# Kernel tuning notes

Measured on AMD Instinct MI355X. Metric: run time of the kernel, lower is better.

The kernel has to match this reference:

```python
import jax, jax.numpy as jnp
import numpy as np

NUM_HEADS = 16

def setup_inputs() -> dict:
    key = jax.random.key(0)
    k1, k2 = jax.random.split(key)
    x = jax.random.normal(k1, (4, 4096, 1024), dtype=jnp.float32)
    # nn.Linear(dim, 3*dim, bias=False) weight: [3*dim, dim]
    w_qkv = jax.random.normal(k2, (3072, 1024), dtype=jnp.float32) * (1024 ** -0.5)
    return {"x": x, "w_qkv": w_qkv}

def reference(x, w_qkv):
    B, N, C = x.shape
    H = NUM_HEADS
    d = C // H
    # qkv projection: [B,N,3C] -> [3,B,H,N,d]
    qkv = jnp.einsum('bnc,oc->bno', x, w_qkv)
    qkv = qkv.reshape(B, N, 3, H, d).transpose(2, 0, 3, 1, 4)
    q, k, v = qkv[0], qkv[1], qkv[2]
    q = jax.nn.softmax(q, axis=-1) * (d ** -0.5)  # softmax over head_dim, then scale
    k = jax.nn.softmax(k, axis=-2)                # softmax over sequence dim
    context = jnp.einsum('bhnd,bhne->bhde', k, v)  # [B,H,d,d]
    out = jnp.einsum('bhnd,bhde->bhne', q, context)  # [B,H,N,d]
    return out
```

## Files before the change

### kernel.cpp

```cpp
#include <hip/hip_runtime.h>
#include <stdint.h>

typedef __attribute__((ext_vector_type(4))) float f32x4;
typedef __attribute__((ext_vector_type(8))) __bf16 bf16x8;
typedef unsigned short u16;

#define AS1 __attribute__((address_space(1)))
#define AS3 __attribute__((address_space(3)))

__device__ __forceinline__ u16 f2bf(float f) {
  uint32_t u = __float_as_uint(f);
  u += 0x7fffu + ((u >> 16) & 1u);
  return (u16)(u >> 16);
}
__device__ __forceinline__ float bf2f(u16 s) {
  return __uint_as_float(((uint32_t)s) << 16);
}

__device__ __forceinline__ void gload_lds16(const void* g, void* l) {
  __builtin_amdgcn_global_load_lds((const AS1 void*)g, (AS3 void*)l, 16, 0, 0);
}

__device__ __forceinline__ bf16x8 ones_bf16x8() {
  uint32_t o4[4] = {0x3F803F80u, 0x3F803F80u, 0x3F803F80u, 0x3F803F80u};
  return *(bf16x8*)o4;
}


__global__ __launch_bounds__(256) void cvt_all(const float* __restrict__ X,
                                               const float* __restrict__ W,
                                               u16* __restrict__ x16,
                                               u16* __restrict__ w16,
                                               float* __restrict__ ctxbase) {
  const int gb = blockIdx.x;
  if (gb >= 9728) {
    const int idx = (gb - 9728) * 256 + threadIdx.x;
    for (int i = idx; i < 66560; i += 1024)
      ((f32x4*)ctxbase)[i] = (f32x4){0.f, 0.f, 0.f, 0.f};
    return;
  }
  const float* src;
  u16* dst;
  int i;
  if (gb < 8192) {
    src = X; dst = x16; i = gb * 256 + threadIdx.x;
  } else {
    src = W; dst = w16; i = (gb - 8192) * 256 + threadIdx.x;
  }
  const f32x4 a = ((const f32x4*)src)[2 * i];
  const f32x4 b = ((const f32x4*)src)[2 * i + 1];
  ushort4 lo, hi;
  lo.x = f2bf(a.x); lo.y = f2bf(a.y); lo.z = f2bf(a.z); lo.w = f2bf(a.w);
  hi.x = f2bf(b.x); hi.y = f2bf(b.y); hi.z = f2bf(b.z); hi.w = f2bf(b.w);
  ((ushort4*)dst)[2 * i] = lo;
  ((ushort4*)dst)[2 * i + 1] = hi;
}

__global__ __launch_bounds__(512, 2) void qkv_gemm(const u16* __restrict__ X,
                                                   const u16* __restrict__ W,
                                                   float* __restrict__ QOUT,
                                                   u16* __restrict__ KV) {
  __shared__ __attribute__((aligned(16))) u16 lds[8 * 128 * 64];

  const int t = threadIdx.x;
  const int D = blockIdx.x;
  const int xcd = D & 7;
  const int s = D >> 3;
  const int otile = s % 12;
  const int mtile = (s / 12) * 8 + xcd;
  const int oblk = otile << 8;
  const int mblk = mtile << 8;

  const int wv = t >> 6;
  const int l = t & 63;
  const int wm = wv >> 2;
  const int wnx = wv & 3;
  const int l15 = l & 15;
  const int lq = l >> 4;
  const int sp = t & 7;

  char* ldsc = (char*)lds;

  auto stageA = [&](int tau, int h, int par) {
#pragma unroll
    for (int j = 0; j < 2; j++) {
      const int ur = (j << 6) | (t >> 3);
      const int R = ((ur >> 6) << 7) | (h << 6) | (ur & 63);
      const u16* g = X + (size_t)(mblk + R) * 1024 + (tau << 6) +
                     ((sp ^ (ur & 7)) << 3);
      gload_lds16(g, ldsc + (((par << 2) | h) << 14) + (((j << 9) | t) << 4));
    }
  };
  auto stageB = [&](int tau, int h, int par) {
#pragma unroll
    for (int j = 0; j < 2; j++) {
      const int ur = (j << 6) | (t >> 3);
      const int R = ((ur >> 5) << 6) | (h << 5) | (ur & 31);
      const u16* g = W + (size_t)(oblk + R) * 1024 + (tau << 6) +
                     ((sp ^ (ur & 7)) << 3);
      gload_lds16(g,
                  ldsc + (((par << 2) | 2 | h) << 14) + (((j << 9) | t) << 4));
    }
  };

  const int co0 = (((l >> 4) ^ (l & 7)) << 4);
  const int co1 = ((((l >> 4) | 4) ^ (l & 7)) << 4);
  const int aOff = ((wm << 6) | l15) << 7;
  const int bOff = ((wnx << 5) | l15) << 7;

  bf16x8 bA[2][4], bL[2][2], bH[2][2];
  auto loadA = [&](int h, int par) {
    const char* base = ldsc + (((par << 2) | h) << 14) + aOff;
#pragma unroll
    for (int fm = 0; fm < 4; fm++) {
      bA[0][fm] = *(const bf16x8*)(base + (fm << 11) + co0);
      bA[1][fm] = *(const bf16x8*)(base + (fm << 11) + co1);
    }
  };
  auto loadB2 = [&](int nh, int par, bf16x8(&bb)[2][2]) {
    const char* base = ldsc + (((par << 2) | 2 | nh) << 14) + bOff;
#pragma unroll
    for (int fn = 0; fn < 2; fn++) {
      bb[0][fn] = *(const bf16x8*)(base + (fn << 11) + co0);
      bb[1][fn] = *(const bf16x8*)(base + (fn << 11) + co1);
    }
  };

  f32x4 acc[8][4];
#pragma unroll
  for (int i = 0; i < 8; i++)
#pragma unroll
    for (int j = 0; j < 4; j++) acc[i][j] = (f32x4){0.f, 0.f, 0.f, 0.f};

  auto mfma16 = [&](int ah, int nh, bf16x8(&bb)[2][2]) {
#pragma unroll
    for (int fm = 0; fm < 4; fm++)
#pragma unroll
      for (int fn = 0; fn < 2; fn++)
#pragma unroll
        for (int ks = 0; ks < 2; ks++)
          acc[(ah << 2) | fm][(nh << 1) | fn] =
              __builtin_amdgcn_mfma_f32_16x16x32_bf16(
                  bA[ks][fm], bb[ks][fn], acc[(ah << 2) | fm][(nh << 1) | fn],
                  0, 0, 0);
  };

  stageA(0, 0, 0);
  stageA(0, 1, 0);
  stageB(0, 0, 0);
  stageB(0, 1, 0);
  stageA(1, 0, 1);
  stageB(1, 1, 1);
  asm volatile("s_waitcnt vmcnt(4)" ::: "memory");
  __builtin_amdgcn_s_barrier();

#pragma unroll 1
  for (int tau = 0; tau < 16; tau++) {
    const int par = tau & 1;
    loadA(0, par);
    loadB2(0, par, bL);
    if (tau < 15) stageA(tau + 1, 1, par ^ 1);
    asm volatile("s_waitcnt lgkmcnt(0)" ::: "memory");
    __builtin_amdgcn_s_setprio(1);
    mfma16(0, 0, bL);
    __builtin_amdgcn_s_setprio(0);
    __builtin_amdgcn_s_barrier();
    loadB2(1, par, bH);
    if (tau < 15) stageB(tau + 1, 0, par ^ 1);
    asm volatile("s_waitcnt lgkmcnt(0)" ::: "memory");
    __builtin_amdgcn_s_setprio(1);
    mfma16(0, 1, bH);
    __builtin_amdgcn_s_setprio(0);
    __builtin_amdgcn_s_barrier();
    loadA(1, par);
    if (tau < 14) stageA(tau + 2, 0, par);
    asm volatile("s_waitcnt lgkmcnt(0)" ::: "memory");
    __builtin_amdgcn_s_setprio(1);
    mfma16(1, 1, bH);
    __builtin_amdgcn_s_setprio(0);
    __builtin_amdgcn_s_barrier();
    if (tau < 14) stageB(tau + 2, 1, par);
    __builtin_amdgcn_s_setprio(1);
    mfma16(1, 0, bL);
    __builtin_amdgcn_s_setprio(0);
    if (tau < 14) {
      asm volatile("s_waitcnt vmcnt(4)" ::: "memory");
    } else if (tau == 14) {
      asm volatile("s_waitcnt vmcnt(0)" ::: "memory");
    }
    __builtin_amdgcn_s_barrier();
  }

  const bool is_q = (oblk < 1024);
  if (is_q) {
    float* LF = (float*)lds;
#pragma unroll 1
    for (int hh = 0; hh < 2; hh++) {
      __syncthreads();
      if (wm == hh) {
#pragma unroll
        for (int fm = 0; fm < 8; fm++) {
#pragma unroll
          for (int fn = 0; fn < 4; fn++) {
            const int colq = ((wnx << 2) | fn);
#pragma unroll
            for (int r = 0; r < 4; r++) {
              const int row = (fm << 4) + (lq << 2) + r;
              const int g = colq ^ lq;
              LF[(row << 8) + (g << 4) + l15] = acc[fm][fn][r];
            }
          }
        }
      }
      __syncthreads();
      const int nbase = mblk + (hh << 7);
#pragma unroll
      for (int p = 0; p < 16; p++) {
        const int u = (p << 9) + t;
        const int row = u >> 6;
        const int c = u & 63;
        const int g = (c >> 2) ^ ((row >> 2) & 3);
        const f32x4 v4 = *(const f32x4*)&LF[(row << 8) + (g << 4) + ((c & 3) << 2)];
        const int rowg = nbase + row;
        const int bq = rowg >> 12, n = rowg & 4095;
        const int head = (oblk >> 6) + (c >> 4);
        *(f32x4*)&QOUT[((((size_t)((bq << 4) + head)) << 12) + n) * 64 +
                       ((c & 15) << 2)] = v4;
      }
    }
  } else {
    u16* ks = KV + (((size_t)((mtile << 3) + (otile - 4))) << 16) + (wv << 13) +
              (l << 2);
#pragma unroll
    for (int fm = 0; fm < 8; fm++) {
#pragma unroll
      for (int fn = 0; fn < 4; fn++) {
        ushort4 sv;
        sv.x = f2bf(acc[fm][fn][0]);
        sv.y = f2bf(acc[fm][fn][1]);
        sv.z = f2bf(acc[fm][fn][2]);
        sv.w = f2bf(acc[fm][fn][3]);
        *(ushort4*)(ks + (((fm << 2) | fn) << 8)) = sv;
      }
    }
  }
}

__global__ __launch_bounds__(256) void ctx_colsum(const u16* __restrict__ KV,
                                                  float* __restrict__ ctxraw,
                                                  float* __restrict__ colsum) {
  __shared__ __attribute__((aligned(16))) u16 ekT[64 * 128];
  __shared__ __attribute__((aligned(16))) u16 evT[64 * 128];

  const int t = threadIdx.x;
  const int bh = blockIdx.y;
  const int b = bh >> 4, h = bh & 15;
  const int sgrp = blockIdx.x;
  const int w = t >> 6;
  const int l = t & 63;
  const int l15 = l & 15;
  const int lk = l >> 4;
  const int lq = (t >> 4) & 3;
  const int d_st = (w << 4) | l15;

  uint2 kr[8], vr[8];
  auto issue = [&](int it) {
    const int mt = (b << 4) + (sgrp << 2) + (it >> 1);
    const int wmb = it & 1;
    const size_t base = ((size_t)((mt << 3) + (h >> 2)) << 16) |
                        ((size_t)wmb << 15) | ((size_t)(h & 3) << 13) |
                        (size_t)(t << 2);
#pragma unroll
    for (int fm = 0; fm < 8; fm++) {
      kr[fm] = *(const uint2*)(KV + base + (fm << 10));
      vr[fm] = *(const uint2*)(KV + base + (fm << 10) + (4 << 16));
    }
  };
  auto stage = [&]() {
#pragma unroll
    for (int fm = 0; fm < 8; fm++) {
      const int c = (fm << 1) | (lq >> 1);
      const int off = (d_st << 8) + ((c ^ (d_st & 7)) << 4) + ((lq & 1) << 3);
      ushort4 es;
      es.x = f2bf(__expf(bf2f((u16)(kr[fm].x & 0xffff))));
      es.y = f2bf(__expf(bf2f((u16)(kr[fm].x >> 16))));
      es.z = f2bf(__expf(bf2f((u16)(kr[fm].y & 0xffff))));
      es.w = f2bf(__expf(bf2f((u16)(kr[fm].y >> 16))));
      *(ushort4*)((char*)ekT + off) = es;
      *(uint2*)((char*)evT + off) = vr[fm];
    }
  };

  f32x4 acc[4], acc1[4];
#pragma unroll
  for (int i = 0; i < 4; i++) {
    acc[i] = (f32x4){0.f, 0.f, 0.f, 0.f};
    acc1[i] = (f32x4){0.f, 0.f, 0.f, 0.f};
  }
  const bf16x8 ones = ones_bf16x8();
  const int eo = (w << 4) | l15;

  issue(0);
#pragma unroll 1
  for (int it = 0; it < 8; it++) {
    stage();
    if (it < 7) issue(it + 1);
    __syncthreads();
#pragma unroll
    for (int ksx = 0; ksx < 4; ksx++) {
      const bf16x8 bfrag = *(const bf16x8*)(
          (char*)evT + (eo << 8) + ((((ksx << 2) | lk) ^ (eo & 7)) << 4));
#pragma unroll
      for (int fmA = 0; fmA < 4; fmA++) {
        const int dA = (fmA << 4) | l15;
        const bf16x8 afrag = *(const bf16x8*)(
            (char*)ekT + (dA << 8) + ((((ksx << 2) | lk) ^ (dA & 7)) << 4));
        acc[fmA] = __builtin_amdgcn_mfma_f32_16x16x32_bf16(afrag, bfrag,
                                                           acc[fmA], 0, 0, 0);
        if (w == 0)
          acc1[fmA] = __builtin_amdgcn_mfma_f32_16x16x32_bf16(afrag, ones,
                                                              acc1[fmA], 0, 0, 0);
      }
    }
    __syncthreads();
  }

  float* dst = ctxraw + ((size_t)bh << 12);
#pragma unroll
  for (int fmA = 0; fmA < 4; fmA++)
#pragma unroll
    for (int r = 0; r < 4; r++) {
      const int d = (fmA << 4) + (lk << 2) + r;
      atomicAdd(&dst[(d << 6) + eo], acc[fmA][r]);
    }
  if (w == 0 && l15 == 0) {
#pragma unroll
    for (int fmA = 0; fmA < 4; fmA++)
#pragma unroll
      for (int r = 0; r < 4; r++) {
        const int d = (fmA << 4) + (lk << 2) + r;
        atomicAdd(&colsum[(bh << 6) + d], acc1[fmA][r]);
      }
  }
}

__global__ __launch_bounds__(256) void out_kernel(const float* __restrict__ ctxraw,
                                                  const float* __restrict__ colsum,
                                                  float* __restrict__ OUT) {
  __shared__ __attribute__((aligned(16))) u16 qe[256 * 64];
  __shared__ __attribute__((aligned(16))) u16 ctxT[64 * 64];

  const int t = threadIdx.x;
  const int bh = blockIdx.y;
  const int n0 = blockIdx.x << 8;
  const float* craw = ctxraw + ((size_t)bh << 12);
  float* qbase = OUT + ((size_t)bh * 4096 + n0) * 64;

#pragma unroll
  for (int p = 0; p < 4; p++) {
    const int vi = (p << 8) + t;
    const int d = vi >> 4;
    const int e4 = (vi & 15) << 2;
    const f32x4 cv = *(const f32x4*)(craw + (vi << 2));
    const float inv = 1.0f / colsum[(bh << 6) + d];
#pragma unroll
    for (int j = 0; j < 4; j++) {
      const int e = e4 + j;
      *(u16*)((char*)ctxT + (e << 7) + (((d >> 3) ^ (e & 7)) << 4) +
              ((d & 7) << 1)) = f2bf(cv[j] * inv);
    }
  }
#pragma unroll
  for (int p = 0; p < 16; p++) {
    const int idx = (p << 8) + t;
    const int row = idx >> 4;
    const int c4 = idx & 15;
    const f32x4 qv = *(const f32x4*)(qbase + (row << 6) + (c4 << 2));
    ushort4 ev;
    ev.x = f2bf(__expf(qv.x));
    ev.y = f2bf(__expf(qv.y));
    ev.z = f2bf(__expf(qv.z));
    ev.w = f2bf(__expf(qv.w));
    *(ushort4*)((char*)qe + (row << 7) + (((c4 >> 1) ^ (row & 7)) << 4) +
                ((c4 & 1) << 3)) = ev;
  }
  __syncthreads();

  const int w = t >> 6;
  const int l = t & 63;
  const int l15 = l & 15;
  const int lk = l >> 4;

  f32x4 acc[4][4], acc1[4];
#pragma unroll
  for (int i = 0; i < 4; i++) {
    acc1[i] = (f32x4){0.f, 0.f, 0.f, 0.f};
#pragma unroll
    for (int j = 0; j < 4; j++) acc[i][j] = (f32x4){0.f, 0.f, 0.f, 0.f};
  }
  const bf16x8 ones = ones_bf16x8();

#pragma unroll
  for (int ksx = 0; ksx < 2; ksx++) {
    bf16x8 bfr[4];
#pragma unroll
    for (int fn = 0; fn < 4; fn++) {
      const int e = (fn << 4) | l15;
      bfr[fn] = *(const bf16x8*)((char*)ctxT + (e << 7) +
                                 ((((ksx << 2) | lk) ^ (e & 7)) << 4));
    }
#pragma unroll
    for (int fm = 0; fm < 4; fm++) {
      const int row = (w << 6) | (fm << 4) | l15;
      const bf16x8 afr = *(const bf16x8*)(
          (char*)qe + (row << 7) + ((((ksx << 2) | lk) ^ (row & 7)) << 4));
      acc1[fm] = __builtin_amdgcn_mfma_f32_16x16x32_bf16(afr, ones, acc1[fm],
                                                         0, 0, 0);
#pragma unroll
      for (int fn = 0; fn < 4; fn++)
        acc[fm][fn] = __builtin_amdgcn_mfma_f32_16x16x32_bf16(afr, bfr[fn],
                                                              acc[fm][fn], 0, 0, 0);
    }
  }

#pragma unroll
  for (int fm = 0; fm < 4; fm++) {
#pragma unroll
    for (int r = 0; r < 4; r++) {
      const int row = (w << 6) + (fm << 4) + (lk << 2) + r;
      const float inv = 0.125f / acc1[fm][r];
#pragma unroll
      for (int fn = 0; fn < 4; fn++)
        qbase[(row << 6) + (fn << 4) + l15] = acc[fm][fn][r] * inv;
    }
  }
}

extern "C" void kernel_launch(void* const* d_in, const int* in_sizes, int n_in,
                              void* d_out, int out_size, void* d_ws, size_t ws_size,
                              hipStream_t stream) {
  const float* Xf = (const float*)d_in[0];
  const float* Wf = (const float*)d_in[1];

  u16* x16 = (u16*)d_ws;
  u16* w16 = x16 + (size_t)16384 * 1024;
  u16* KV = w16 + (size_t)3072 * 1024;
  float* ctxraw = (float*)(KV + (size_t)16384 * 2048);
  float* colsum = ctxraw + 64 * 64 * 64;
  float* QOUT = (float*)d_out;

  cvt_all<<<dim3(9732), 256, 0, stream>>>(Xf, Wf, x16, w16, ctxraw);
  qkv_gemm<<<dim3(768), 512, 0, stream>>>(x16, w16, QOUT, KV);
  ctx_colsum<<<dim3(4, 64), 256, 0, stream>>>(KV, ctxraw, colsum);
  out_kernel<<<dim3(16, 64), 256, 0, stream>>>(ctxraw, colsum, QOUT);
}
```

Measured before the change: 264.7 us.

## Load GEMM B operand directly from global into registers, halve LDS footprint

The QKV GEMM no longer stages the weight tile through LDS. Each wave now loads its B fragments straight from global memory into registers, and only the X tile is double-buffered in shared memory, which halves the LDS allocation. The main loop drops most of its barriers and waits. The Q epilogue is reorganized into four 64-row passes so it fits the smaller LDS. The aim is more occupancy and less LDS traffic and synchronization, at the cost of uncoalesced, unswizzled global loads for W and a full vmcnt(0) wait every iteration, which exposes latency.

```diff
diff --git a/kernel.cpp b/kernel.cpp
--- a/kernel.cpp
+++ b/kernel.cpp
@@ -60,7 +60,7 @@
                                                    const u16* __restrict__ W,
                                                    float* __restrict__ QOUT,
                                                    u16* __restrict__ KV) {
-  __shared__ __attribute__((aligned(16))) u16 lds[8 * 128 * 64];
+  __shared__ __attribute__((aligned(16))) u16 lds[4 * 128 * 64];
 
   const int t = threadIdx.x;
   const int D = blockIdx.x;
@@ -88,41 +88,30 @@
       const int R = ((ur >> 6) << 7) | (h << 6) | (ur & 63);
       const u16* g = X + (size_t)(mblk + R) * 1024 + (tau << 6) +
                      ((sp ^ (ur & 7)) << 3);
-      gload_lds16(g, ldsc + (((par << 2) | h) << 14) + (((j << 9) | t) << 4));
-    }
-  };
-  auto stageB = [&](int tau, int h, int par) {
-#pragma unroll
-    for (int j = 0; j < 2; j++) {
-      const int ur = (j << 6) | (t >> 3);
-      const int R = ((ur >> 5) << 6) | (h << 5) | (ur & 31);
-      const u16* g = W + (size_t)(oblk + R) * 1024 + (tau << 6) +
-                     ((sp ^ (ur & 7)) << 3);
-      gload_lds16(g,
-                  ldsc + (((par << 2) | 2 | h) << 14) + (((j << 9) | t) << 4));
-    }
+      gload_lds16(g, ldsc + (((par << 1) | h) << 14) + (((j << 9) | t) << 4));
+    }
+  };
+
+  auto loadBg = [&](int tau, int nh, bf16x8(&bb)[2][2]) {
+    const u16* base = W + (size_t)(oblk + (wnx << 6) + (nh << 5) + l15) * 1024 +
+                      (tau << 6) + (lq << 3);
+    bb[0][0] = *(const bf16x8*)(base);
+    bb[0][1] = *(const bf16x8*)(base + 16 * 1024);
+    bb[1][0] = *(const bf16x8*)(base + 32);
+    bb[1][1] = *(const bf16x8*)(base + 16 * 1024 + 32);
   };
 
   const int co0 = (((l >> 4) ^ (l & 7)) << 4);
   const int co1 = ((((l >> 4) | 4) ^ (l & 7)) << 4);
   const int aOff = ((wm << 6) | l15) << 7;
-  const int bOff = ((wnx << 5) | l15) << 7;
 
   bf16x8 bA[2][4], bL[2][2], bH[2][2];
   auto loadA = [&](int h, int par) {
-    const char* base = ldsc + (((par << 2) | h) << 14) + aOff;
+    const char* base = ldsc + (((par << 1) | h) << 14) + aOff;
 #pragma unroll
     for (int fm = 0; fm < 4; fm++) {
       bA[0][fm] = *(const bf16x8*)(base + (fm << 11) + co0);
       bA[1][fm] = *(const bf16x8*)(base + (fm << 11) + co1);
-    }
-  };
-  auto loadB2 = [&](int nh, int par, bf16x8(&bb)[2][2]) {
-    const char* base = ldsc + (((par << 2) | 2 | nh) << 14) + bOff;
-#pragma unroll
-    for (int fn = 0; fn < 2; fn++) {
-      bb[0][fn] = *(const bf16x8*)(base + (fn << 11) + co0);
-      bb[1][fn] = *(const bf16x8*)(base + (fn << 11) + co1);
     }
   };
 
@@ -147,47 +136,32 @@
 
   stageA(0, 0, 0);
   stageA(0, 1, 0);
-  stageB(0, 0, 0);
-  stageB(0, 1, 0);
-  stageA(1, 0, 1);
-  stageB(1, 1, 1);
-  asm volatile("s_waitcnt vmcnt(4)" ::: "memory");
+  loadBg(0, 0, bL);
+  asm volatile("s_waitcnt vmcnt(0)" ::: "memory");
   __builtin_amdgcn_s_barrier();
 
 #pragma unroll 1
   for (int tau = 0; tau < 16; tau++) {
     const int par = tau & 1;
+    if (tau < 15) {
+      stageA(tau + 1, 0, par ^ 1);
+      stageA(tau + 1, 1, par ^ 1);
+    }
+    loadBg(tau, 1, bH);
     loadA(0, par);
-    loadB2(0, par, bL);
-    if (tau < 15) stageA(tau + 1, 1, par ^ 1);
-    asm volatile("s_waitcnt lgkmcnt(0)" ::: "memory");
     __builtin_amdgcn_s_setprio(1);
     mfma16(0, 0, bL);
-    __builtin_amdgcn_s_setprio(0);
-    __builtin_amdgcn_s_barrier();
-    loadB2(1, par, bH);
-    if (tau < 15) stageB(tau + 1, 0, par ^ 1);
-    asm volatile("s_waitcnt lgkmcnt(0)" ::: "memory");
-    __builtin_amdgcn_s_setprio(1);
     mfma16(0, 1, bH);
     __builtin_amdgcn_s_setprio(0);
-    __builtin_amdgcn_s_barrier();
     loadA(1, par);
-    if (tau < 14) stageA(tau + 2, 0, par);
-    asm volatile("s_waitcnt lgkmcnt(0)" ::: "memory");
+    __builtin_amdgcn_s_setprio(1);
+    mfma16(1, 0, bL);
+    __builtin_amdgcn_s_setprio(0);
+    if (tau < 15) loadBg(tau + 1, 0, bL);
     __builtin_amdgcn_s_setprio(1);
     mfma16(1, 1, bH);
     __builtin_amdgcn_s_setprio(0);
-    __builtin_amdgcn_s_barrier();
-    if (tau < 14) stageB(tau + 2, 1, par);
-    __builtin_amdgcn_s_setprio(1);
-    mfma16(1, 0, bL);
-    __builtin_amdgcn_s_setprio(0);
-    if (tau < 14) {
-      asm volatile("s_waitcnt vmcnt(4)" ::: "memory");
-    } else if (tau == 14) {
-      asm volatile("s_waitcnt vmcnt(0)" ::: "memory");
-    }
+    asm volatile("s_waitcnt vmcnt(0)" ::: "memory");
     __builtin_amdgcn_s_barrier();
   }
 
@@ -195,28 +169,29 @@
   if (is_q) {
     float* LF = (float*)lds;
 #pragma unroll 1
-    for (int hh = 0; hh < 2; hh++) {
+    for (int p = 0; p < 4; p++) {
       __syncthreads();
-      if (wm == hh) {
-#pragma unroll
-        for (int fm = 0; fm < 8; fm++) {
+      if (wm == (p >> 1)) {
+#pragma unroll
+        for (int jf = 0; jf < 4; jf++) {
+          const int j = ((p & 1) << 2) + jf;
 #pragma unroll
           for (int fn = 0; fn < 4; fn++) {
             const int colq = ((wnx << 2) | fn);
 #pragma unroll
             for (int r = 0; r < 4; r++) {
-              const int row = (fm << 4) + (lq << 2) + r;
+              const int rl = (jf << 4) + (lq << 2) + r;
               const int g = colq ^ lq;
-              LF[(row << 8) + (g << 4) + l15] = acc[fm][fn][r];
+              LF[(rl << 8) + (g << 4) + l15] = acc[j][fn][r];
             }
           }
         }
       }
       __syncthreads();
-      const int nbase = mblk + (hh << 7);
-#pragma unroll
-      for (int p = 0; p < 16; p++) {
-        const int u = (p << 9) + t;
+      const int nbase = mblk + (wm == 0 ? 0 : 0) + (p << 6);
+#pragma unroll
+      for (int p8 = 0; p8 < 8; p8++) {
+        const int u = (p8 << 9) + t;
         const int row = u >> 6;
         const int c = u & 63;
         const int g = (c >> 2) ^ ((row >> 2) & 3);
```

New measurement: 388.4 us. +46.8%, slower.
